# Kernel optimization log

Hardware: AMD Instinct MI355X
Metric: run time of the kernel (lower is better)

## Reference

```python
import jax, jax.numpy as jnp
import numpy as np


def _dct_basis(n: int) -> jnp.ndarray:
    # Unnormalized DCT-II basis matching torch_dct.dct(norm=None):
    # X[k] = 2 * sum_n x[n] * cos(pi*(2n+1)*k / (2N))
    k = np.arange(n)[:, None]
    m = np.arange(n)[None, :]
    D = 2.0 * np.cos(np.pi * (2.0 * m + 1.0) * k / (2.0 * n))
    return jnp.asarray(D, dtype=jnp.float32)


def setup_inputs() -> dict:
    key = jax.random.key(0)
    img = jax.random.normal(key, (32, 3, 512, 512), dtype=jnp.float32)
    return {"img": img}


def reference(img) -> jnp.ndarray:
    B, C, H, W = img.shape
    Dh = _dct_basis(H)  # [H, H]
    Dw = _dct_basis(W)  # [W, W]
    x = img.astype(jnp.float32)
    # 2D DCT-II: Dh @ x @ Dw^T, batched over (B, C); fused /1000 scale.
    tmp = jnp.einsum('kh,bchw->bckw', Dh, x)
    out = jnp.einsum('bckw,lw->bckl', tmp, Dw) / 1000.0
    return out
```

## Files before the change

### kernel.cpp

```cpp
#include <hip/hip_runtime.h>
#include <hip/hip_bf16.h>
#include <stdint.h>

#define NPIX 512
#define NBC  96
#define NWG8 (NBC * 4)

typedef __attribute__((ext_vector_type(8))) short bf16x8;
typedef __attribute__((ext_vector_type(4))) float f32x4;
typedef __attribute__((ext_vector_type(8))) unsigned short u16x8;

__device__ __forceinline__ unsigned short f2bf(float f) {
    __hip_bfloat16 h = __float2bfloat16(f);
    union { __hip_bfloat16 h; unsigned short u; } v;
    v.h = h;
    return v.u;
}

#define GLD16(g, l) __builtin_amdgcn_global_load_lds( \
    (const __attribute__((address_space(1))) void*)(const void*)(g), \
    (__attribute__((address_space(3))) void*)(void*)(l), 16, 0, 0)

#define SBAR() do { __builtin_amdgcn_sched_barrier(0); \
                    __builtin_amdgcn_s_barrier(); \
                    __builtin_amdgcn_sched_barrier(0); } while (0)
#define LGKM0() do { asm volatile("s_waitcnt lgkmcnt(0)" ::: "memory"); \
                     __builtin_amdgcn_sched_barrier(0); } while (0)
#define SB0() __builtin_amdgcn_sched_barrier(0)

__global__ void k_basis(unsigned short* __restrict__ D) {
    int idx = blockIdx.x * 256 + threadIdx.x;
    int k = idx >> 9, n = idx & 511;
    int m = ((2 * n + 1) * k) & 2047;
    float ang = (float)m * 3.06796157577128218e-03f;
    D[idx] = f2bf(2.0f * cosf(ang));
}

__global__ __launch_bounds__(512) void k_s1fused(
        const float* __restrict__ X,
        const unsigned short* __restrict__ D,
        unsigned short* __restrict__ sT) {
    __shared__ __align__(16) char LDS[131072];

    const int bid = blockIdx.x;
    const int nb  = (bid & 7) * (NWG8 / 8) + (bid >> 3);
    const int bc = nb >> 2, mt = (nb >> 1) & 1, nt = nb & 1;
    const int mA0 = mt * 256, nB0 = nt * 256;
    const float* Ximg = X + (size_t)bc * NPIX * NPIX;

    const int tid  = threadIdx.x;
    const int lane = tid & 63;
    const int wid  = tid >> 6;
    const int wr = wid >> 2, wc = wid & 3;
    const int rm = lane & 15;
    const int kq = lane >> 4;

    const int rpA = tid >> 2, qA = tid & 3;
    const int rowLocalBase = ((rpA >> 6) << 7) + (rpA & 63);

    f32x4 acc[8][4] = {};
    bf16x8 a[4][2], b0[2][2], b1[2][2];
    float4 av0[4], av1[4];

    auto issueA = [&](int kt, int H, float4 (&av)[4]) {
        const float* src = Ximg + (size_t)(mA0 + rowLocalBase + H * 64) * NPIX
                                + kt * 64 + qA * 16;
        av[0] = *(const float4*)(src + 0);
        av[1] = *(const float4*)(src + 4);
        av[2] = *(const float4*)(src + 8);
        av[3] = *(const float4*)(src + 12);
    };
    auto writeAh = [&](int p, int H, float4 (&av)[4]) {
        char* dst = LDS + p * 32768 + H * 16384 + rpA * 128;
        u16x8 w0, w1;
        w0[0] = f2bf(av[0].x); w0[1] = f2bf(av[0].y); w0[2] = f2bf(av[0].z); w0[3] = f2bf(av[0].w);
        w0[4] = f2bf(av[1].x); w0[5] = f2bf(av[1].y); w0[6] = f2bf(av[1].z); w0[7] = f2bf(av[1].w);
        w1[0] = f2bf(av[2].x); w1[1] = f2bf(av[2].y); w1[2] = f2bf(av[2].z); w1[3] = f2bf(av[2].w);
        w1[4] = f2bf(av[3].x); w1[5] = f2bf(av[3].y); w1[6] = f2bf(av[3].z); w1[7] = f2bf(av[3].w);
        *(u16x8*)(dst + (((qA * 2 + 0) ^ (rpA & 7)) * 16)) = w0;
        *(u16x8*)(dst + (((qA * 2 + 1) ^ (rpA & 7)) * 16)) = w1;
    };
    auto stageBg = [&](int kt, int p, int H) {
        char* dst = LDS + 65536 + p * 32768 + H * 16384;
        #pragma unroll
        for (int it = 0; it < 2; ++it) {
            int c = it * 512 + tid;
            int rp = c >> 3, g = c & 7;
            int gs = g ^ (rp & 7);
            int row = ((rp >> 5) << 6) + H * 32 + (rp & 31);
            GLD16(D + (size_t)(nB0 + row) * NPIX + kt * 64 + gs * 8, dst + c * 16);
        }
    };
    auto readA = [&](int p, int mh) {
        const char* base = LDS + p * 32768 + mh * 16384;
        #pragma unroll
        for (int f = 0; f < 4; ++f) {
            int rp = wr * 64 + f * 16 + rm;
            #pragma unroll
            for (int ks = 0; ks < 2; ++ks) {
                int slot = (ks * 4 + kq) ^ (rm & 7);
                a[f][ks] = *(const bf16x8*)(base + rp * 128 + slot * 16);
            }
        }
    };
    auto readB = [&](int p, int nh, bf16x8 (&b)[2][2]) {
        const char* base = LDS + 65536 + p * 32768 + nh * 16384;
        #pragma unroll
        for (int jj = 0; jj < 2; ++jj) {
            int rp = wc * 32 + jj * 16 + rm;
            #pragma unroll
            for (int ks = 0; ks < 2; ++ks) {
                int slot = (ks * 4 + kq) ^ (rm & 7);
                b[jj][ks] = *(const bf16x8*)(base + rp * 128 + slot * 16);
            }
        }
    };
    auto mma = [&](int mh, int nh, bf16x8 (&b)[2][2]) {
        __builtin_amdgcn_s_setprio(1);
        #pragma unroll
        for (int f = 0; f < 4; ++f)
            #pragma unroll
            for (int jj = 0; jj < 2; ++jj)
                #pragma unroll
                for (int ks = 0; ks < 2; ++ks)
                    acc[mh * 4 + f][nh * 2 + jj] = __builtin_amdgcn_mfma_f32_16x16x32_bf16(
                        a[f][ks], b[jj][ks], acc[mh * 4 + f][nh * 2 + jj], 0, 0, 0);
        __builtin_amdgcn_s_setprio(0);
    };

    issueA(0, 0, av0); SB0();
    stageBg(0, 0, 0);  SB0();
    issueA(0, 1, av1); SB0();
    stageBg(0, 0, 1);  SB0();
    asm volatile("s_waitcnt vmcnt(8)" ::: "memory"); SB0();
    writeAh(0, 0, av0);
    asm volatile("s_waitcnt vmcnt(2)" ::: "memory"); SB0();
    writeAh(0, 1, av1);

    for (int T = 0; T < 7; ++T) {
        const int p = T & 1, pn = p ^ 1;
        asm volatile("s_waitcnt lgkmcnt(0)" ::: "memory");
        SBAR();
        readA(p, 0); readB(p, 0, b0);
        issueA(T + 1, 0, av0); SB0();
        stageBg(T + 1, pn, 0); SB0();
        LGKM0(); mma(0, 0, b0);
        asm volatile("s_waitcnt vmcnt(6)" ::: "memory");
        SBAR();
        readB(p, 1, b1);
        issueA(T + 1, 1, av1); SB0();
        stageBg(T + 1, pn, 1); SB0();
        LGKM0(); mma(0, 1, b1);
        asm volatile("s_waitcnt vmcnt(8)" ::: "memory");
        SBAR();
        readA(p, 1);
        LGKM0();
        writeAh(pn, 0, av0); SB0();
        mma(1, 0, b0);
        asm volatile("s_waitcnt vmcnt(2)" ::: "memory");
        asm volatile("s_waitcnt lgkmcnt(0)" ::: "memory");
        SBAR();
        writeAh(pn, 1, av1); SB0();
        mma(1, 1, b1);
    }
    {
        asm volatile("s_waitcnt lgkmcnt(0)" ::: "memory");
        SBAR();
        readA(1, 0); readB(1, 0, b0); LGKM0(); mma(0, 0, b0);
        asm volatile("s_waitcnt vmcnt(0)" ::: "memory");
        SBAR();
        readB(1, 1, b1); LGKM0(); mma(0, 1, b1);
        SBAR();
        readA(1, 1); LGKM0(); mma(1, 0, b0);
        SBAR();
        mma(1, 1, b1);
    }

    SBAR();
    #pragma unroll
    for (int mh = 0; mh < 2; ++mh)
        #pragma unroll
        for (int f = 0; f < 4; ++f) {
            int h_loc = wr * 128 + mh * 64 + f * 16 + kq * 4;
            #pragma unroll
            for (int nh = 0; nh < 2; ++nh)
                #pragma unroll
                for (int jj = 0; jj < 2; ++jj) {
                    int l_loc = wc * 64 + (nh * 2 + jj) * 16 + rm;
                    int byte = (l_loc * 512 + h_loc * 2) ^ ((l_loc & 7) << 4);
                    f32x4 v = acc[mh * 4 + f][nh * 2 + jj];
                    ushort4 w;
                    w.x = f2bf(v[0]); w.y = f2bf(v[1]);
                    w.z = f2bf(v[2]); w.w = f2bf(v[3]);
                    *(ushort4*)(LDS + byte) = w;
                }
        }
    LGKM0(); SBAR();
    unsigned short* Co = sT + (size_t)bc * NPIX * NPIX;
    #pragma unroll
    for (int i = 0; i < 16; ++i) {
        int chunk = i * 512 + tid;
        int l_loc = chunk >> 5, g = chunk & 31;
        int byte = (l_loc * 512 + g * 16) ^ ((l_loc & 7) << 4);
        u16x8 v = *(const u16x8*)(LDS + byte);
        *(u16x8*)&Co[(size_t)(nB0 + l_loc) * NPIX + mA0 + g * 8] = v;
    }
}

__global__ __launch_bounds__(512) void k_gemm8(
        const unsigned short* __restrict__ A, size_t strideA,
        const unsigned short* __restrict__ B, size_t strideB,
        float* __restrict__ Cv) {
    __shared__ __align__(16) char LDS[131072];

    const int bid = blockIdx.x;
    const int nb  = (bid & 7) * (NWG8 / 8) + (bid >> 3);
    const int bc = nb >> 2, mt = (nb >> 1) & 1, nt = nb & 1;
    const int mA0 = mt * 256, nB0 = nt * 256;
    const unsigned short* Aimg = A + (size_t)bc * strideA;
    const unsigned short* Bimg = B + (size_t)bc * strideB;

    const int tid  = threadIdx.x;
    const int lane = tid & 63;
    const int wid  = tid >> 6;
    const int wr = wid >> 2, wc = wid & 3;
    const int rm = lane & 15;
    const int kq = lane >> 4;

    f32x4 acc[8][4] = {};
    bf16x8 a[4][2], b0[2][2], b1[2][2];

    auto stageA = [&](int kt, int p, int H) {
        char* dst = LDS + p * 32768 + H * 16384;
        #pragma unroll
        for (int it = 0; it < 2; ++it) {
            int c = it * 512 + tid;
            int rp = c >> 3, g = c & 7;
            int gs = g ^ (rp & 7);
            int row = ((rp >> 6) << 7) + H * 64 + (rp & 63);
            GLD16(Aimg + (size_t)(mA0 + row) * NPIX + kt * 64 + gs * 8, dst + c * 16);
        }
    };
    auto stageB = [&](int kt, int p, int H) {
        char* dst = LDS + 65536 + p * 32768 + H * 16384;
        #pragma unroll
        for (int it = 0; it < 2; ++it) {
            int c = it * 512 + tid;
            int rp = c >> 3, g = c & 7;
            int gs = g ^ (rp & 7);
            int row = ((rp >> 5) << 6) + H * 32 + (rp & 31);
            GLD16(Bimg + (size_t)(nB0 + row) * NPIX + kt * 64 + gs * 8, dst + c * 16);
        }
    };
    auto readA = [&](int p, int mh) {
        const char* base = LDS + p * 32768 + mh * 16384;
        #pragma unroll
        for (int f = 0; f < 4; ++f) {
            int rp = wr * 64 + f * 16 + rm;
            #pragma unroll
            for (int ks = 0; ks < 2; ++ks) {
                int slot = (ks * 4 + kq) ^ (rm & 7);
                a[f][ks] = *(const bf16x8*)(base + rp * 128 + slot * 16);
            }
        }
    };
    auto readB = [&](int p, int nh, bf16x8 (&b)[2][2]) {
        const char* base = LDS + 65536 + p * 32768 + nh * 16384;
        #pragma unroll
        for (int jj = 0; jj < 2; ++jj) {
            int rp = wc * 32 + jj * 16 + rm;
            #pragma unroll
            for (int ks = 0; ks < 2; ++ks) {
                int slot = (ks * 4 + kq) ^ (rm & 7);
                b[jj][ks] = *(const bf16x8*)(base + rp * 128 + slot * 16);
            }
        }
    };
    auto mma = [&](int mh, int nh, bf16x8 (&b)[2][2]) {
        __builtin_amdgcn_s_setprio(1);
        #pragma unroll
        for (int f = 0; f < 4; ++f)
            #pragma unroll
            for (int jj = 0; jj < 2; ++jj)
                #pragma unroll
                for (int ks = 0; ks < 2; ++ks)
                    acc[mh * 4 + f][nh * 2 + jj] = __builtin_amdgcn_mfma_f32_16x16x32_bf16(
                        a[f][ks], b[jj][ks], acc[mh * 4 + f][nh * 2 + jj], 0, 0, 0);
        __builtin_amdgcn_s_setprio(0);
    };

    stageA(0, 0, 0); stageB(0, 0, 0); stageB(0, 0, 1); stageA(0, 0, 1);

    for (int T = 0; T < 7; ++T) {
        const int p = T & 1, pn = p ^ 1;
        asm volatile("s_waitcnt vmcnt(4)" ::: "memory"); SBAR();
        readA(p, 0); readB(p, 0, b0); stageA(T + 1, pn, 0);
        LGKM0(); mma(0, 0, b0);
        asm volatile("s_waitcnt vmcnt(4)" ::: "memory"); SBAR();
        readB(p, 1, b1); stageB(T + 1, pn, 0);
        LGKM0(); mma(0, 1, b1);
        asm volatile("s_waitcnt vmcnt(4)" ::: "memory"); SBAR();
        readA(p, 1); stageB(T + 1, pn, 1);
        LGKM0(); mma(1, 0, b0);
        SBAR();
        stageA(T + 1, pn, 1);
        mma(1, 1, b1);
    }
    {
        asm volatile("s_waitcnt vmcnt(4)" ::: "memory"); SBAR();
        readA(1, 0); readB(1, 0, b0); LGKM0(); mma(0, 0, b0);
        asm volatile("s_waitcnt vmcnt(2)" ::: "memory"); SBAR();
        readB(1, 1, b1); LGKM0(); mma(0, 1, b1);
        asm volatile("s_waitcnt vmcnt(0)" ::: "memory"); SBAR();
        readA(1, 1); LGKM0(); mma(1, 0, b0);
        SBAR();
        mma(1, 1, b1);
    }

    float* Co = Cv + (size_t)bc * NPIX * NPIX;
    #pragma unroll
    for (int mh = 0; mh < 2; ++mh)
        #pragma unroll
        for (int f = 0; f < 4; ++f) {
            int k_ = mA0 + wr * 128 + mh * 64 + f * 16 + kq * 4;
            #pragma unroll
            for (int nh = 0; nh < 2; ++nh)
                #pragma unroll
                for (int jj = 0; jj < 2; ++jj) {
                    int l_ = nB0 + wc * 64 + (nh * 2 + jj) * 16 + rm;
                    f32x4 v = acc[mh * 4 + f][nh * 2 + jj];
                    #pragma unroll
                    for (int r = 0; r < 4; ++r)
                        Co[(size_t)(k_ + r) * NPIX + l_] = v[r] * 1.0e-3f;
                }
        }
}

extern "C" void kernel_launch(void* const* d_in, const int* in_sizes, int n_in,
                              void* d_out, int out_size, void* d_ws, size_t ws_size,
                              hipStream_t stream) {
    const float* img = (const float*)d_in[0];
    float* out = (float*)d_out;

    unsigned short* D  = (unsigned short*)d_ws;
    unsigned short* sT = (unsigned short*)((char*)d_ws + 512 * 1024);

    k_basis<<<dim3(512 * 512 / 256), dim3(256), 0, stream>>>(D);

    k_s1fused<<<dim3(NWG8), dim3(512), 0, stream>>>(img, D, sT);

    k_gemm8<<<dim3(NWG8), dim3(512), 0, stream>>>(
        D, 0, sT, (size_t)NPIX * NPIX, out);
}
```

Baseline: 99.14 us.

## Split fp32-to-bf16 conversion into a separate pass and stage both GEMM operands via LDS DMA

Adds a standalone kernel that converts the fp32 image to bf16 in a workspace buffer, or in the output buffer when the workspace is too small. The first GEMM stage then loads both operands with global_load_lds DMA instead of register loads followed by conversion and LDS writes, and its pipeline wait counts are reworked. This removes conversion work and VGPR pressure from the GEMM main loop. The cost is an extra full read and write pass over the image (about 100MB fp32 read plus 50MB bf16 write) and one more launch.

```diff
diff --git a/kernel.cpp b/kernel.cpp
--- a/kernel.cpp
+++ b/kernel.cpp
@@ -26,7 +26,6 @@
                     __builtin_amdgcn_sched_barrier(0); } while (0)
 #define LGKM0() do { asm volatile("s_waitcnt lgkmcnt(0)" ::: "memory"); \
                      __builtin_amdgcn_sched_barrier(0); } while (0)
-#define SB0() __builtin_amdgcn_sched_barrier(0)
 
 __global__ void k_basis(unsigned short* __restrict__ D) {
     int idx = blockIdx.x * 256 + threadIdx.x;
@@ -36,8 +35,23 @@
     D[idx] = f2bf(2.0f * cosf(ang));
 }
 
-__global__ __launch_bounds__(512) void k_s1fused(
-        const float* __restrict__ X,
+__global__ __launch_bounds__(256) void k_cvt(const float* __restrict__ X,
+                                             unsigned short* __restrict__ Xbf) {
+    size_t t = (size_t)blockIdx.x * 256 + threadIdx.x;
+    const float4* src = (const float4*)X + t * 4;
+    float4 a = src[0], b = src[1], c = src[2], d = src[3];
+    u16x8 w0, w1;
+    w0[0] = f2bf(a.x); w0[1] = f2bf(a.y); w0[2] = f2bf(a.z); w0[3] = f2bf(a.w);
+    w0[4] = f2bf(b.x); w0[5] = f2bf(b.y); w0[6] = f2bf(b.z); w0[7] = f2bf(b.w);
+    w1[0] = f2bf(c.x); w1[1] = f2bf(c.y); w1[2] = f2bf(c.z); w1[3] = f2bf(c.w);
+    w1[4] = f2bf(d.x); w1[5] = f2bf(d.y); w1[6] = f2bf(d.z); w1[7] = f2bf(d.w);
+    u16x8* dst = (u16x8*)Xbf + t * 2;
+    dst[0] = w0;
+    dst[1] = w1;
+}
+
+__global__ __launch_bounds__(512) void k_s1g(
+        const unsigned short* __restrict__ Xbf,
         const unsigned short* __restrict__ D,
         unsigned short* __restrict__ sT) {
     __shared__ __align__(16) char LDS[131072];
@@ -46,7 +60,8 @@
     const int nb  = (bid & 7) * (NWG8 / 8) + (bid >> 3);
     const int bc = nb >> 2, mt = (nb >> 1) & 1, nt = nb & 1;
     const int mA0 = mt * 256, nB0 = nt * 256;
-    const float* Ximg = X + (size_t)bc * NPIX * NPIX;
+    const unsigned short* Aimg = Xbf + (size_t)bc * NPIX * NPIX;
+    const unsigned short* Bimg = D;
 
     const int tid  = threadIdx.x;
     const int lane = tid & 63;
@@ -55,32 +70,21 @@
     const int rm = lane & 15;
     const int kq = lane >> 4;
 
-    const int rpA = tid >> 2, qA = tid & 3;
-    const int rowLocalBase = ((rpA >> 6) << 7) + (rpA & 63);
-
     f32x4 acc[8][4] = {};
     bf16x8 a[4][2], b0[2][2], b1[2][2];
-    float4 av0[4], av1[4];
-
-    auto issueA = [&](int kt, int H, float4 (&av)[4]) {
-        const float* src = Ximg + (size_t)(mA0 + rowLocalBase + H * 64) * NPIX
-                                + kt * 64 + qA * 16;
-        av[0] = *(const float4*)(src + 0);
-        av[1] = *(const float4*)(src + 4);
-        av[2] = *(const float4*)(src + 8);
-        av[3] = *(const float4*)(src + 12);
-    };
-    auto writeAh = [&](int p, int H, float4 (&av)[4]) {
-        char* dst = LDS + p * 32768 + H * 16384 + rpA * 128;
-        u16x8 w0, w1;
-        w0[0] = f2bf(av[0].x); w0[1] = f2bf(av[0].y); w0[2] = f2bf(av[0].z); w0[3] = f2bf(av[0].w);
-        w0[4] = f2bf(av[1].x); w0[5] = f2bf(av[1].y); w0[6] = f2bf(av[1].z); w0[7] = f2bf(av[1].w);
-        w1[0] = f2bf(av[2].x); w1[1] = f2bf(av[2].y); w1[2] = f2bf(av[2].z); w1[3] = f2bf(av[2].w);
-        w1[4] = f2bf(av[3].x); w1[5] = f2bf(av[3].y); w1[6] = f2bf(av[3].z); w1[7] = f2bf(av[3].w);
-        *(u16x8*)(dst + (((qA * 2 + 0) ^ (rpA & 7)) * 16)) = w0;
-        *(u16x8*)(dst + (((qA * 2 + 1) ^ (rpA & 7)) * 16)) = w1;
-    };
-    auto stageBg = [&](int kt, int p, int H) {
+
+    auto stageA = [&](int kt, int p, int H) {
+        char* dst = LDS + p * 32768 + H * 16384;
+        #pragma unroll
+        for (int it = 0; it < 2; ++it) {
+            int c = it * 512 + tid;
+            int rp = c >> 3, g = c & 7;
+            int gs = g ^ (rp & 7);
+            int row = ((rp >> 6) << 7) + H * 64 + (rp & 63);
+            GLD16(Aimg + (size_t)(mA0 + row) * NPIX + kt * 64 + gs * 8, dst + c * 16);
+        }
+    };
+    auto stageB = [&](int kt, int p, int H) {
         char* dst = LDS + 65536 + p * 32768 + H * 16384;
         #pragma unroll
         for (int it = 0; it < 2; ++it) {
@@ -88,7 +92,7 @@
             int rp = c >> 3, g = c & 7;
             int gs = g ^ (rp & 7);
             int row = ((rp >> 5) << 6) + H * 32 + (rp & 31);
-            GLD16(D + (size_t)(nB0 + row) * NPIX + kt * 64 + gs * 8, dst + c * 16);
+            GLD16(Bimg + (size_t)(nB0 + row) * NPIX + kt * 64 + gs * 8, dst + c * 16);
         }
     };
     auto readA = [&](int p, int mh) {
@@ -128,49 +132,29 @@
         __builtin_amdgcn_s_setprio(0);
     };
 
-    issueA(0, 0, av0); SB0();
-    stageBg(0, 0, 0);  SB0();
-    issueA(0, 1, av1); SB0();
-    stageBg(0, 0, 1);  SB0();
-    asm volatile("s_waitcnt vmcnt(8)" ::: "memory"); SB0();
-    writeAh(0, 0, av0);
-    asm volatile("s_waitcnt vmcnt(2)" ::: "memory"); SB0();
-    writeAh(0, 1, av1);
+    stageA(0, 0, 0); stageB(0, 0, 0); stageB(0, 0, 1); stageA(0, 0, 1);
 
     for (int T = 0; T < 7; ++T) {
         const int p = T & 1, pn = p ^ 1;
-        asm volatile("s_waitcnt lgkmcnt(0)" ::: "memory");
+        asm volatile("s_waitcnt vmcnt(4)" ::: "memory"); SBAR();
+        readA(p, 0); readB(p, 0, b0); stageA(T + 1, pn, 0);
+        LGKM0(); mma(0, 0, b0);
+        asm volatile("s_waitcnt vmcnt(4)" ::: "memory"); SBAR();
+        readB(p, 1, b1); stageB(T + 1, pn, 0);
+        LGKM0(); mma(0, 1, b1);
+        asm volatile("s_waitcnt vmcnt(4)" ::: "memory"); SBAR();
+        readA(p, 1); stageB(T + 1, pn, 1);
+        LGKM0(); mma(1, 0, b0);
         SBAR();
-        readA(p, 0); readB(p, 0, b0);
-        issueA(T + 1, 0, av0); SB0();
-        stageBg(T + 1, pn, 0); SB0();
-        LGKM0(); mma(0, 0, b0);
-        asm volatile("s_waitcnt vmcnt(6)" ::: "memory");
-        SBAR();
-        readB(p, 1, b1);
-        issueA(T + 1, 1, av1); SB0();
-        stageBg(T + 1, pn, 1); SB0();
-        LGKM0(); mma(0, 1, b1);
-        asm volatile("s_waitcnt vmcnt(8)" ::: "memory");
-        SBAR();
-        readA(p, 1);
-        LGKM0();
-        writeAh(pn, 0, av0); SB0();
-        mma(1, 0, b0);
-        asm volatile("s_waitcnt vmcnt(2)" ::: "memory");
-        asm volatile("s_waitcnt lgkmcnt(0)" ::: "memory");
-        SBAR();
-        writeAh(pn, 1, av1); SB0();
+        stageA(T + 1, pn, 1);
         mma(1, 1, b1);
     }
     {
-        asm volatile("s_waitcnt lgkmcnt(0)" ::: "memory");
-        SBAR();
+        asm volatile("s_waitcnt vmcnt(4)" ::: "memory"); SBAR();
         readA(1, 0); readB(1, 0, b0); LGKM0(); mma(0, 0, b0);
-        asm volatile("s_waitcnt vmcnt(0)" ::: "memory");
-        SBAR();
+        asm volatile("s_waitcnt vmcnt(2)" ::: "memory"); SBAR();
         readB(1, 1, b1); LGKM0(); mma(0, 1, b1);
-        SBAR();
+        asm volatile("s_waitcnt vmcnt(0)" ::: "memory"); SBAR();
         readA(1, 1); LGKM0(); mma(1, 0, b0);
         SBAR();
         mma(1, 1, b1);
@@ -207,9 +191,9 @@
     }
 }
 
-__global__ __launch_bounds__(512) void k_gemm8(
-        const unsigned short* __restrict__ A, size_t strideA,
-        const unsigned short* __restrict__ B, size_t strideB,
+__global__ __launch_bounds__(512) void k_s2g(
+        const unsigned short* __restrict__ D,
+        const unsigned short* __restrict__ sT,
         float* __restrict__ Cv) {
     __shared__ __align__(16) char LDS[131072];
 
@@ -217,8 +201,8 @@
     const int nb  = (bid & 7) * (NWG8 / 8) + (bid >> 3);
     const int bc = nb >> 2, mt = (nb >> 1) & 1, nt = nb & 1;
     const int mA0 = mt * 256, nB0 = nt * 256;
-    const unsigned short* Aimg = A + (size_t)bc * strideA;
-    const unsigned short* Bimg = B + (size_t)bc * strideB;
+    const unsigned short* Aimg = D;
+    const unsigned short* Bimg = sT + (size_t)bc * NPIX * NPIX;
 
     const int tid  = threadIdx.x;
     const int lane = tid & 63;
@@ -342,13 +326,21 @@
     const float* img = (const float*)d_in[0];
     float* out = (float*)d_out;
 
+    const size_t ST_OFF = 512 * 1024;
+    const size_t ST_SZ  = (size_t)NBC * NPIX * NPIX * 2;
+    const size_t XBF_SZ = ST_SZ;
+
     unsigned short* D  = (unsigned short*)d_ws;
-    unsigned short* sT = (unsigned short*)((char*)d_ws + 512 * 1024);
+    unsigned short* sT = (unsigned short*)((char*)d_ws + ST_OFF);
+    unsigned short* Xbf;
+    if (ws_size >= ST_OFF + ST_SZ + XBF_SZ)
+        Xbf = (unsigned short*)((char*)d_ws + ST_OFF + ST_SZ);
+    else
+        Xbf = (unsigned short*)d_out;
 
     k_basis<<<dim3(512 * 512 / 256), dim3(256), 0, stream>>>(D);
-
-    k_s1fused<<<dim3(NWG8), dim3(512), 0, stream>>>(img, D, sT);
-
-    k_gemm8<<<dim3(NWG8), dim3(512), 0, stream>>>(
-        D, 0, sT, (size_t)NPIX * NPIX, out);
-}
+    k_cvt<<<dim3((int)((size_t)NBC * NPIX * NPIX / 16 / 256)), dim3(256), 0, stream>>>(img, Xbf);
+
+    k_s1g<<<dim3(NWG8), dim3(512), 0, stream>>>(Xbf, D, sT);
+    k_s2g<<<dim3(NWG8), dim3(512), 0, stream>>>(D, sT, out);
+}
```

Result: slower. 111.1 us (+12.0%).
